# Optimization experiments

Measured on AMD Instinct MI355X. Metric: run time of the kernel, lower is better.

Reference implementation:

```python
import jax, jax.numpy as jnp
import numpy as np

N, E, D_IN, HID, OUT, EDIM, L, NT, ET = 50000, 800000, 128, 128, 128, 32, 3, 2, 3
PUMP = 1
LN_EPS = 1e-5


def setup_inputs() -> dict:
    key = jax.random.key(0)
    ks = jax.random.split(key, 12)
    s = 0.05
    x = jax.random.normal(ks[0], (N, D_IN), jnp.float32)
    edge_index = jax.random.randint(ks[1], (2, E), 0, N, dtype=jnp.int64)
    edge_attr = jax.random.normal(ks[2], (E, EDIM), jnp.float32)
    node_type = jax.random.randint(ks[3], (N,), 0, NT, dtype=jnp.int64)
    edge_type = jax.random.randint(ks[4], (E,), 0, ET, dtype=jnp.int64)
    # per-layer HydroConv params
    node_W = jax.random.normal(ks[5], (L, NT, HID, D_IN), jnp.float32) * s   # per-node-type Linear weight
    node_b = jax.random.normal(ks[6], (L, NT, HID), jnp.float32) * s
    edge_W = jax.random.normal(ks[7], (L, ET, 2, EDIM), jnp.float32) * s     # out dim padded to 2; row 1 only used for pump type
    edge_b = jax.random.normal(ks[8], (L, ET, 2), jnp.float32) * s
    emb = jax.random.normal(ks[9], (L, ET, EDIM), jnp.float32) * s           # edge_type_emb per layer
    ln_g = jnp.ones((L, HID), jnp.float32)
    ln_b = jnp.zeros((L, HID), jnp.float32)
    fc_W = jax.random.normal(ks[10], (OUT, HID), jnp.float32) * s
    fc_b = jnp.zeros((OUT,), jnp.float32)
    return dict(x=x, edge_attr=edge_attr, node_W=node_W, node_b=node_b,
                edge_W=edge_W, edge_b=edge_b, emb=emb, ln_g=ln_g, ln_b=ln_b,
                fc_W=fc_W, fc_b=fc_b, edge_index=edge_index,
                node_type=node_type, edge_type=edge_type)


def _hydro_conv(h, edge_index, edge_attr, node_type, edge_type, nW, nb, eW, eb, emb_l):
    src, dst = edge_index[0], edge_index[1]           # x_j = h[src], x_i = h[dst]
    direction = edge_attr[:, -2:-1]                    # [E,1]
    pump = edge_attr[:, -1:]                           # [E,1]
    ea = edge_attr + emb_l[edge_type]                  # [E,EDIM]
    raw = jnp.einsum('ec,toc->eto', ea, eW) + eb       # [E,ET,2]
    raw = jnp.take_along_axis(raw, edge_type[:, None, None], axis=1)[:, 0]  # [E,2] per-edge-type MLP
    gain = jax.nn.softplus(raw[:, :1])                 # [E,1]
    speed = pump * jnp.where(direction > 0, direction, jnp.ones_like(direction))
    is_pump = (edge_type == PUMP)[:, None]
    gain = jnp.where(is_pump, gain * speed, gain)
    bias = jnp.where(is_pump, raw[:, 1:2] * speed, jnp.zeros_like(gain))
    sign = direction * 2.0 - 1.0
    msg = sign * (gain * (h[src] - h[dst]) + bias)     # [E,C]
    aggr = jax.ops.segment_sum(msg, dst, num_segments=N)  # scatter-add to target nodes
    out = jnp.zeros((N, nW.shape[1]), h.dtype)
    for t in range(NT):                                # per-node-type Linear
        ht = aggr @ nW[t].T + nb[t]
        out = jnp.where((node_type == t)[:, None], ht, out)
    return out


def reference(x, edge_attr, node_W, node_b, edge_W, edge_b, emb, ln_g, ln_b,
              fc_W, fc_b, edge_index, node_type, edge_type):
    h = x
    for l in range(L):
        identity = h
        h = _hydro_conv(h, edge_index, edge_attr, node_type, edge_type,
                        node_W[l], node_b[l], edge_W[l], edge_b[l], emb[l])
        h = jax.nn.relu(h)
        mu = jnp.mean(h, axis=-1, keepdims=True)
        var = jnp.mean(jnp.square(h - mu), axis=-1, keepdims=True)
        h = (h - mu) * jax.lax.rsqrt(var + LN_EPS) * ln_g[l] + ln_b[l]
        if identity.shape == h.shape:                  # residual
            h = h + identity
    return h @ fc_W.T + fc_b
```

## Files before the change

### kernel.cpp

```cpp
#include <hip/hip_runtime.h>
#include <math.h>

#define NN 50000
#define EE 800000
#define D 128
#define EDIM 32
#define LL 3
#define NT 2
#define ET 3
#define NB 196
#define NPAD 50080
#define NTILE 1565
#define NBLKM 392

typedef _Float16 f16x8 __attribute__((ext_vector_type(8)));
typedef float f32x4 __attribute__((ext_vector_type(4)));

__device__ __forceinline__ void cvt8(const float4 u, const float4 v, f16x8& hi, f16x8& lo) {
    float x[8] = {u.x, u.y, u.z, u.w, v.x, v.y, v.z, v.w};
#pragma unroll
    for (int e = 0; e < 8; e++) {
        _Float16 h = (_Float16)x[e];
        hi[e] = h;
        lo[e] = (_Float16)(x[e] - (float)h);
    }
}

__global__ __launch_bounds__(256) void k_pcount(const int* __restrict__ nt, int* __restrict__ pc) {
    __shared__ int s[256];
    int d = blockIdx.x * 256 + threadIdx.x;
    int ind = 0;
    if (d < NN) ind = (nt[d] == 0) ? 1 : 0x10000;
    s[threadIdx.x] = ind;
    __syncthreads();
    for (int st = 128; st; st >>= 1) {
        if (threadIdx.x < st) s[threadIdx.x] += s[threadIdx.x + st];
        __syncthreads();
    }
    if (threadIdx.x == 0) pc[blockIdx.x] = s[0];
}

__global__ __launch_bounds__(256) void k_pscan(const int* __restrict__ pc, int* __restrict__ po,
                                               int* __restrict__ meta) {
    __shared__ int s[256];
    int t = threadIdx.x;
    int v = (t < NB) ? pc[t] : 0;
    s[t] = v;
    __syncthreads();
    for (int st = 1; st < 256; st <<= 1) {
        int add = (t >= st) ? s[t - st] : 0;
        __syncthreads();
        s[t] += add;
        __syncthreads();
    }
    if (t < NB) po[t] = s[t] - v;
    if (t == 0) {
        int tot = s[255];
        meta[3] = ((tot & 0xffff) + 63) & ~63;
    }
}

__global__ __launch_bounds__(256) void k_passign(const int* __restrict__ nt, const int* __restrict__ po,
                                                 const int* __restrict__ meta,
                                                 int* __restrict__ pos, int* __restrict__ inv) {
    __shared__ int s[256];
    int t = threadIdx.x;
    int d = blockIdx.x * 256 + t;
    int ty = (d < NN) ? nt[d] : -1;
    int ind = (ty == 0) ? 1 : ((ty == 1) ? 0x10000 : 0);
    s[t] = ind;
    __syncthreads();
    for (int st = 1; st < 256; st <<= 1) {
        int add = (t >= st) ? s[t - st] : 0;
        __syncthreads();
        s[t] += add;
        __syncthreads();
    }
    if (d >= NN) return;
    int excl = s[t] - ind;
    int pop = po[blockIdx.x];
    int p;
    if (ty == 0) p = (pop & 0xffff) + (excl & 0xffff);
    else         p = meta[3] + (pop >> 16) + (excl >> 16);
    pos[d] = p;
    inv[p] = d;
}

__global__ __launch_bounds__(256) void k_permx(const float* __restrict__ x, const int* __restrict__ pos,
                                               float* __restrict__ h0) {
    int flat = blockIdx.x * 256 + threadIdx.x;
    if (flat >= NN * 32) return;
    int d = flat >> 5, f4 = flat & 31;
    int p = pos[d];
    ((float4*)h0)[(size_t)p * 32 + f4] = ((const float4*)x)[(size_t)d * 32 + f4];
}

__global__ __launch_bounds__(256) void k_hist(const int* __restrict__ dst, int* __restrict__ deg) {
    int e = blockIdx.x * 256 + threadIdx.x;
    if (e < EE) atomicAdd(&deg[dst[e]], 1);
}

__global__ __launch_bounds__(256) void k_scan_bsum(const int* __restrict__ deg, int* __restrict__ bsum) {
    __shared__ int s[256];
    int t = threadIdx.x;
    int d = blockIdx.x * 256 + t;
    s[t] = (d < NN) ? deg[d] : 0;
    __syncthreads();
    for (int st = 128; st > 0; st >>= 1) {
        if (t < st) s[t] += s[t + st];
        __syncthreads();
    }
    if (t == 0) bsum[blockIdx.x] = s[0];
}

__global__ __launch_bounds__(256) void k_scan_boff(const int* __restrict__ bsum, int* __restrict__ boff) {
    __shared__ int s[256];
    int t = threadIdx.x;
    s[t] = (t < NB) ? bsum[t] : 0;
    __syncthreads();
    for (int st = 1; st < 256; st <<= 1) {
        int add = (t >= st) ? s[t - st] : 0;
        __syncthreads();
        s[t] += add;
        __syncthreads();
    }
    if (t < NB) boff[t] = (t == 0) ? 0 : s[t - 1];
}

__global__ __launch_bounds__(256) void k_scan_offs(const int* __restrict__ deg, const int* __restrict__ boff,
                                                   int* __restrict__ offs, int* __restrict__ cur) {
    __shared__ int s[256];
    int t = threadIdx.x;
    int d = blockIdx.x * 256 + t;
    int v = (d < NN) ? deg[d] : 0;
    s[t] = v;
    __syncthreads();
    for (int st = 1; st < 256; st <<= 1) {
        int add = (t >= st) ? s[t - st] : 0;
        __syncthreads();
        s[t] += add;
        __syncthreads();
    }
    if (d < NN) {
        int excl = s[t] - v + boff[blockIdx.x];
        offs[d] = excl;
        cur[d]  = excl;
    }
}

__global__ __launch_bounds__(256) void k_edge(const float* __restrict__ edge_attr,
                                              const float* __restrict__ edge_W,
                                              const float* __restrict__ edge_b,
                                              const float* __restrict__ emb,
                                              const int* __restrict__ ei,
                                              const int* __restrict__ etype,
                                              const int* __restrict__ pos,
                                              int* __restrict__ cur,
                                              float4* __restrict__ esort) {
    __shared__ float eWl[LL * ET * 2 * EDIM];
    __shared__ float ebd[LL * ET * 2];
    int t0 = threadIdx.x;
    for (int i = t0; i < LL * ET * 2 * EDIM; i += 256) eWl[i] = edge_W[i];
    __syncthreads();
    if (t0 < LL * ET * 2) {
        int l = t0 / (ET * 2);
        int rem = t0 % (ET * 2);
        int tt = rem / 2;
        float sum = edge_b[t0];
        const float* em = emb + (l * ET + tt) * EDIM;
        const float* w  = eWl + t0 * EDIM;
        for (int c = 0; c < EDIM; c++) sum += em[c] * w[c];
        ebd[t0] = sum;
    }
    __syncthreads();
    int e = blockIdx.x * 256 + t0;
    if (e >= EE) return;

    float a[EDIM];
    const float4* ap = (const float4*)(edge_attr + (size_t)e * EDIM);
#pragma unroll
    for (int i = 0; i < EDIM / 4; i++) {
        float4 v = ap[i];
        a[4 * i + 0] = v.x; a[4 * i + 1] = v.y; a[4 * i + 2] = v.z; a[4 * i + 3] = v.w;
    }
    int tt = etype[e];
    float dir  = a[EDIM - 2];
    float pump = a[EDIM - 1];
    float sign = dir * 2.f - 1.f;
    float speed = pump * (dir > 0.f ? dir : 1.f);
    int src = ei[e];
    int dst = ei[EE + e];
    int sp = pos[src];
    int p = atomicAdd(&cur[dst], 1);
    float Av[LL], Bv[LL];
#pragma unroll
    for (int l = 0; l < LL; l++) {
        const float* w0 = eWl + ((l * ET + tt) * 2 + 0) * EDIM;
        const float* w1 = w0 + EDIM;
        float r0 = ebd[(l * ET + tt) * 2 + 0];
        float r1 = ebd[(l * ET + tt) * 2 + 1];
#pragma unroll
        for (int c = 0; c < EDIM; c++) { r0 += a[c] * w0[c]; r1 += a[c] * w1[c]; }
        float gain = fmaxf(r0, 0.f) + log1pf(expf(-fabsf(r0)));
        float bias = 0.f;
        if (tt == 1) { gain *= speed; bias = r1 * speed; }
        Av[l] = sign * gain;
        Bv[l] = sign * bias;
    }
    float4 e0 = make_float4(__int_as_float(sp), Av[0], Av[1], Av[2]);
    float4 e1 = make_float4(Bv[0], Bv[1], Bv[2], 0.f);
    esort[(size_t)p * 2 + 0] = e0;
    esort[(size_t)p * 2 + 1] = e1;
}

__global__ __launch_bounds__(256) void k_gather(const float* __restrict__ h,
                                                const int* __restrict__ offs,
                                                const int* __restrict__ deg,
                                                const int* __restrict__ pos,
                                                const float4* __restrict__ esort,
                                                int layer,
                                                float* __restrict__ aggr) {
    __shared__ float4 rbuf[2][32];
    __shared__ float  rsum[2][2];
    int local = threadIdx.x;
    int nb = local >> 7;
    int node = blockIdx.x * 2 + nb;
    int t = local & 127;
    int w = t >> 5;
    int f4 = t & 31;
    int start = offs[node];
    int n = deg[node];
    int p = pos[node];

    float4 acc = make_float4(0.f, 0.f, 0.f, 0.f);
    float sA = 0.f, sB = 0.f;
    for (int k = w; k < n; k += 4) {
        size_t idx = (size_t)(start + k) * 2;
        float4 e0 = esort[idx];
        float4 e1 = esort[idx + 1];
        int sp = __float_as_int(e0.x);
        float A = (layer == 0) ? e0.y : ((layer == 1) ? e0.z : e0.w);
        float B = (layer == 0) ? e1.x : ((layer == 1) ? e1.y : e1.z);
        float4 hv = *(const float4*)&h[(size_t)sp * D + 4 * f4];
        acc.x += A * hv.x; acc.y += A * hv.y; acc.z += A * hv.z; acc.w += A * hv.w;
        sA += A; sB += B;
    }
    acc.x += __shfl_xor(acc.x, 32); acc.y += __shfl_xor(acc.y, 32);
    acc.z += __shfl_xor(acc.z, 32); acc.w += __shfl_xor(acc.w, 32);
    sA += __shfl_xor(sA, 32); sB += __shfl_xor(sB, 32);
    if (((local >> 6) & 1) == 1 && (t & 63) < 32) {
        rbuf[nb][f4] = acc;
        if (f4 == 0) { rsum[nb][0] = sA; rsum[nb][1] = sB; }
    }
    __syncthreads();
    if (((local >> 6) & 1) == 0 && (t & 63) < 32) {
        float4 o = rbuf[nb][f4];
        float sAt = sA + rsum[nb][0];
        float sBt = sB + rsum[nb][1];
        float4 hd = *(const float4*)&h[(size_t)p * D + 4 * f4];
        float4 r;
        r.x = acc.x + o.x - sAt * hd.x + sBt;
        r.y = acc.y + o.y - sAt * hd.y + sBt;
        r.z = acc.z + o.z - sAt * hd.z + sBt;
        r.w = acc.w + o.w - sAt * hd.w + sBt;
        *(float4*)&aggr[(size_t)p * D + 4 * f4] = r;
    }
}

__global__ __launch_bounds__(256) void k_node(const float* __restrict__ aggr,
                                              const float* __restrict__ hprev,
                                              const float* __restrict__ Wg,
                                              const float* __restrict__ bg,
                                              const float* __restrict__ lng,
                                              const float* __restrict__ lnb,
                                              const int* __restrict__ meta,
                                              float* __restrict__ hnext) {
    int wid  = threadIdx.x >> 6;
    int lane = threadIdx.x & 63;
    int w0 = (blockIdx.x * 4 + wid) * 32;
    if (w0 >= NPAD) return;
    int l15 = lane & 15, lg = lane >> 4;
    int tt = (w0 >= meta[3]) ? 1 : 0;
    const float* W = Wg + (size_t)tt * D * D;

    f32x4 acc[2][8];
#pragma unroll
    for (int i = 0; i < 2; i++)
#pragma unroll
        for (int j = 0; j < 8; j++) acc[i][j] = (f32x4){0.f, 0.f, 0.f, 0.f};

#pragma unroll 1
    for (int ks = 0; ks < 4; ks++) {
        int kb = ks * 32 + 8 * lg;
        float4 rA[2][2], rB[8][2];
#pragma unroll
        for (int i = 0; i < 2; i++) {
            const float* p = aggr + (size_t)(w0 + 16 * i + l15) * D + kb;
            rA[i][0] = *(const float4*)p;
            rA[i][1] = *(const float4*)(p + 4);
        }
#pragma unroll
        for (int j = 0; j < 8; j++) {
            const float* p = W + (size_t)(16 * j + l15) * D + kb;
            rB[j][0] = *(const float4*)p;
            rB[j][1] = *(const float4*)(p + 4);
        }
        f16x8 ahi[2], alo[2];
#pragma unroll
        for (int i = 0; i < 2; i++) cvt8(rA[i][0], rA[i][1], ahi[i], alo[i]);
#pragma unroll
        for (int j = 0; j < 8; j++) {
            f16x8 bhi, blo;
            cvt8(rB[j][0], rB[j][1], bhi, blo);
#pragma unroll
            for (int i = 0; i < 2; i++) {
                acc[i][j] = __builtin_amdgcn_mfma_f32_16x16x32_f16(ahi[i], bhi, acc[i][j], 0, 0, 0);
                acc[i][j] = __builtin_amdgcn_mfma_f32_16x16x32_f16(alo[i], bhi, acc[i][j], 0, 0, 0);
                acc[i][j] = __builtin_amdgcn_mfma_f32_16x16x32_f16(ahi[i], blo, acc[i][j], 0, 0, 0);
            }
        }
    }

    float bv[8], gv[8], bb[8];
#pragma unroll
    for (int j = 0; j < 8; j++) {
        int col = 16 * j + l15;
        bv[j] = bg[tt * D + col];
        gv[j] = lng[col];
        bb[j] = lnb[col];
    }
#pragma unroll
    for (int i = 0; i < 2; i++)
#pragma unroll
        for (int j = 0; j < 8; j++)
#pragma unroll
            for (int r = 0; r < 4; r++)
                acc[i][j][r] = fmaxf(acc[i][j][r] + bv[j], 0.f);

    float mu[2][4], rs[2][4];
#pragma unroll
    for (int i = 0; i < 2; i++)
#pragma unroll
        for (int r = 0; r < 4; r++) {
            float s = 0.f, s2 = 0.f;
#pragma unroll
            for (int j = 0; j < 8; j++) { float v = acc[i][j][r]; s += v; s2 += v * v; }
#pragma unroll
            for (int m = 1; m < 16; m <<= 1) { s += __shfl_xor(s, m); s2 += __shfl_xor(s2, m); }
            float mm = s * (1.f / 128.f);
            mu[i][r] = mm;
            rs[i][r] = rsqrtf(s2 * (1.f / 128.f) - mm * mm + 1e-5f);
        }

#pragma unroll
    for (int i = 0; i < 2; i++)
#pragma unroll
        for (int r = 0; r < 4; r++) {
            int row = w0 + 16 * i + 4 * lg + r;
#pragma unroll
            for (int j = 0; j < 8; j++) {
                int col = 16 * j + l15;
                float v = (acc[i][j][r] - mu[i][r]) * rs[i][r] * gv[j] + bb[j]
                          + hprev[(size_t)row * D + col];
                hnext[(size_t)row * D + col] = v;
            }
        }
}

__global__ __launch_bounds__(256) void k_fc(const float* __restrict__ hin,
                                            const float* __restrict__ W,
                                            const float* __restrict__ bias,
                                            const int* __restrict__ inv,
                                            float* __restrict__ out) {
    int wid  = threadIdx.x >> 6;
    int lane = threadIdx.x & 63;
    int w0 = (blockIdx.x * 4 + wid) * 32;
    if (w0 >= NPAD) return;
    int l15 = lane & 15, lg = lane >> 4;

    f32x4 acc[2][8];
#pragma unroll
    for (int i = 0; i < 2; i++)
#pragma unroll
        for (int j = 0; j < 8; j++) acc[i][j] = (f32x4){0.f, 0.f, 0.f, 0.f};

#pragma unroll 1
    for (int ks = 0; ks < 4; ks++) {
        int kb = ks * 32 + 8 * lg;
        float4 rA[2][2], rB[8][2];
#pragma unroll
        for (int i = 0; i < 2; i++) {
            const float* p = hin + (size_t)(w0 + 16 * i + l15) * D + kb;
            rA[i][0] = *(const float4*)p;
            rA[i][1] = *(const float4*)(p + 4);
        }
#pragma unroll
        for (int j = 0; j < 8; j++) {
            const float* p = W + (size_t)(16 * j + l15) * D + kb;
            rB[j][0] = *(const float4*)p;
            rB[j][1] = *(const float4*)(p + 4);
        }
        f16x8 ahi[2], alo[2];
#pragma unroll
        for (int i = 0; i < 2; i++) cvt8(rA[i][0], rA[i][1], ahi[i], alo[i]);
#pragma unroll
        for (int j = 0; j < 8; j++) {
            f16x8 bhi, blo;
            cvt8(rB[j][0], rB[j][1], bhi, blo);
#pragma unroll
            for (int i = 0; i < 2; i++) {
                acc[i][j] = __builtin_amdgcn_mfma_f32_16x16x32_f16(ahi[i], bhi, acc[i][j], 0, 0, 0);
                acc[i][j] = __builtin_amdgcn_mfma_f32_16x16x32_f16(alo[i], bhi, acc[i][j], 0, 0, 0);
                acc[i][j] = __builtin_amdgcn_mfma_f32_16x16x32_f16(ahi[i], blo, acc[i][j], 0, 0, 0);
            }
        }
    }

    float bv[8];
#pragma unroll
    for (int j = 0; j < 8; j++) bv[j] = bias[16 * j + l15];

#pragma unroll
    for (int i = 0; i < 2; i++)
#pragma unroll
        for (int r = 0; r < 4; r++) {
            int row = w0 + 16 * i + 4 * lg + r;
            int orig = inv[row];
            if (orig >= 0) {
#pragma unroll
                for (int j = 0; j < 8; j++)
                    out[(size_t)orig * D + 16 * j + l15] = acc[i][j][r] + bv[j];
            }
        }
}

extern "C" void kernel_launch(void* const* d_in, const int* in_sizes, int n_in,
                              void* d_out, int out_size, void* d_ws, size_t ws_size,
                              hipStream_t stream) {
    const float* x         = (const float*)d_in[0];
    const float* edge_attr = (const float*)d_in[1];
    const float* node_W    = (const float*)d_in[2];
    const float* node_b    = (const float*)d_in[3];
    const float* edge_W    = (const float*)d_in[4];
    const float* edge_b    = (const float*)d_in[5];
    const float* emb       = (const float*)d_in[6];
    const float* ln_g      = (const float*)d_in[7];
    const float* ln_b      = (const float*)d_in[8];
    const float* fc_W      = (const float*)d_in[9];
    const float* fc_b      = (const float*)d_in[10];
    const int*   edge_index = (const int*)d_in[11];
    const int*   node_type  = (const int*)d_in[12];
    const int*   edge_type  = (const int*)d_in[13];
    float* out = (float*)d_out;

    char* w = (char*)d_ws;
    auto alloc = [&](size_t bytes) {
        void* p = (void*)w;
        w += (bytes + 255) & ~(size_t)255;
        return p;
    };
    float*  P     = (float*)alloc((size_t)NPAD * D * 4);
    float*  Q     = (float*)alloc((size_t)NPAD * D * 4);
    float*  G     = (float*)alloc((size_t)NPAD * D * 4);
    float4* esort = (float4*)alloc((size_t)EE * 32);
    int*    pos   = (int*)alloc((size_t)NN * 4);
    int*    inv   = (int*)alloc((size_t)NPAD * 4);
    int*    deg   = (int*)alloc((size_t)NN * 4);
    int*    offs  = (int*)alloc((size_t)NN * 4);
    int*    cur   = (int*)alloc((size_t)NN * 4);
    int*    bsum  = (int*)alloc(256 * 4);
    int*    boff  = (int*)alloc(256 * 4);
    int*    pc    = (int*)alloc(256 * 4);
    int*    po    = (int*)alloc(256 * 4);
    int*    meta  = (int*)alloc(8 * 4);

    hipMemsetAsync(deg, 0, (size_t)NN * 4, stream);
    hipMemsetAsync(inv, 0xFF, (size_t)NPAD * 4, stream);

    k_pcount<<<NB, 256, 0, stream>>>(node_type, pc);
    k_pscan<<<1, 256, 0, stream>>>(pc, po, meta);
    k_passign<<<NB, 256, 0, stream>>>(node_type, po, meta, pos, inv);
    k_permx<<<(NN * 32 + 255) / 256, 256, 0, stream>>>(x, pos, P);

    k_hist<<<(EE + 255) / 256, 256, 0, stream>>>(edge_index + EE, deg);
    k_scan_bsum<<<NB, 256, 0, stream>>>(deg, bsum);
    k_scan_boff<<<1, 256, 0, stream>>>(bsum, boff);
    k_scan_offs<<<NB, 256, 0, stream>>>(deg, boff, offs, cur);
    k_edge<<<(EE + 255) / 256, 256, 0, stream>>>(edge_attr, edge_W, edge_b, emb,
                                                 edge_index, edge_type, pos, cur, esort);

    const float* hin = P;
    float* outs[LL] = {Q, P, Q};
    for (int l = 0; l < LL; l++) {
        k_gather<<<NN / 2, 256, 0, stream>>>(hin, offs, deg, pos, esort, l, G);
        k_node<<<NBLKM, 256, 0, stream>>>(G, hin,
                                          node_W + (size_t)l * NT * D * D,
                                          node_b + (size_t)l * NT * D,
                                          ln_g + (size_t)l * D,
                                          ln_b + (size_t)l * D,
                                          meta, outs[l]);
        hin = outs[l];
    }
    k_fc<<<NBLKM, 256, 0, stream>>>(hin, fc_W, fc_b, inv, out);
}
```

Before: 595.5 us.

## Split edge sort, use per-layer compact edge arrays, halve MFMA row tiles

Edge sorting is split into a separate atomic scatter of edge ids, then a sorted-order edge kernel that reads attributes through the id indirection. It writes per-layer (src, A) float2 arrays instead of a 32-byte record, and pushes the pump-edge bias into a per-node sum with atomics. The gather reads only 8 bytes per edge and unrolls two edges per iteration to overlap the h loads. The node and fc GEMM kernels move from 32-row to 16-row tiles per wave, launching more blocks with fewer registers. The cost is an extra kernel pass, uncoalesced edge_attr reads, float atomics on the bias sums, and the W tile being loaded more often.

```diff
diff --git a/kernel.cpp b/kernel.cpp
--- a/kernel.cpp
+++ b/kernel.cpp
@@ -10,8 +10,8 @@
 #define ET 3
 #define NB 196
 #define NPAD 50080
-#define NTILE 1565
-#define NBLKM 392
+#define NT16 3130
+#define NBLK16 783
 
 typedef _Float16 f16x8 __attribute__((ext_vector_type(8)));
 typedef float f32x4 __attribute__((ext_vector_type(4)));
@@ -148,33 +148,45 @@
     }
 }
 
-__global__ __launch_bounds__(256) void k_edge(const float* __restrict__ edge_attr,
-                                              const float* __restrict__ edge_W,
-                                              const float* __restrict__ edge_b,
-                                              const float* __restrict__ emb,
-                                              const int* __restrict__ ei,
-                                              const int* __restrict__ etype,
-                                              const int* __restrict__ pos,
-                                              int* __restrict__ cur,
-                                              float4* __restrict__ esort) {
-    __shared__ float eWl[LL * ET * 2 * EDIM];
-    __shared__ float ebd[LL * ET * 2];
+__global__ __launch_bounds__(256) void k_scateid(const int* __restrict__ dst,
+                                                 int* __restrict__ cur, int* __restrict__ eid) {
+    int e = blockIdx.x * 256 + threadIdx.x;
+    if (e < EE) {
+        int d = dst[e];
+        int p = atomicAdd(&cur[d], 1);
+        eid[p] = e;
+    }
+}
+
+__global__ __launch_bounds__(256) void k_edge2(const float* __restrict__ edge_attr,
+                                               const float* __restrict__ edge_W,
+                                               const float* __restrict__ edge_b,
+                                               const float* __restrict__ emb,
+                                               const int* __restrict__ ei,
+                                               const int* __restrict__ etype,
+                                               const int* __restrict__ pos,
+                                               const int* __restrict__ eid,
+                                               float2* __restrict__ spA,
+                                               float* __restrict__ sBn) {
+    __shared__ float eWl[18 * 33];
+    __shared__ float ebd[18];
     int t0 = threadIdx.x;
-    for (int i = t0; i < LL * ET * 2 * EDIM; i += 256) eWl[i] = edge_W[i];
-    __syncthreads();
-    if (t0 < LL * ET * 2) {
+    for (int i = t0; i < 18 * EDIM; i += 256) eWl[(i >> 5) * 33 + (i & 31)] = edge_W[i];
+    __syncthreads();
+    if (t0 < 18) {
         int l = t0 / (ET * 2);
         int rem = t0 % (ET * 2);
         int tt = rem / 2;
         float sum = edge_b[t0];
         const float* em = emb + (l * ET + tt) * EDIM;
-        const float* w  = eWl + t0 * EDIM;
+        const float* w  = eWl + t0 * 33;
         for (int c = 0; c < EDIM; c++) sum += em[c] * w[c];
         ebd[t0] = sum;
     }
     __syncthreads();
-    int e = blockIdx.x * 256 + t0;
-    if (e >= EE) return;
+    int p = blockIdx.x * 256 + t0;
+    if (p >= EE) return;
+    int e = eid[p];
 
     float a[EDIM];
     const float4* ap = (const float4*)(edge_attr + (size_t)e * EDIM);
@@ -189,14 +201,12 @@
     float sign = dir * 2.f - 1.f;
     float speed = pump * (dir > 0.f ? dir : 1.f);
     int src = ei[e];
-    int dst = ei[EE + e];
     int sp = pos[src];
-    int p = atomicAdd(&cur[dst], 1);
     float Av[LL], Bv[LL];
 #pragma unroll
     for (int l = 0; l < LL; l++) {
-        const float* w0 = eWl + ((l * ET + tt) * 2 + 0) * EDIM;
-        const float* w1 = w0 + EDIM;
+        const float* w0 = eWl + ((l * ET + tt) * 2 + 0) * 33;
+        const float* w1 = w0 + 33;
         float r0 = ebd[(l * ET + tt) * 2 + 0];
         float r1 = ebd[(l * ET + tt) * 2 + 1];
 #pragma unroll
@@ -207,21 +217,27 @@
         Av[l] = sign * gain;
         Bv[l] = sign * bias;
     }
-    float4 e0 = make_float4(__int_as_float(sp), Av[0], Av[1], Av[2]);
-    float4 e1 = make_float4(Bv[0], Bv[1], Bv[2], 0.f);
-    esort[(size_t)p * 2 + 0] = e0;
-    esort[(size_t)p * 2 + 1] = e1;
+#pragma unroll
+    for (int l = 0; l < LL; l++)
+        spA[(size_t)l * EE + p] = make_float2(__int_as_float(sp), Av[l]);
+    if (tt == 1) {
+        int dst = ei[EE + e];
+        int pd = pos[dst];
+#pragma unroll
+        for (int l = 0; l < LL; l++) atomicAdd(&sBn[l * NPAD + pd], Bv[l]);
+    }
 }
 
 __global__ __launch_bounds__(256) void k_gather(const float* __restrict__ h,
                                                 const int* __restrict__ offs,
                                                 const int* __restrict__ deg,
                                                 const int* __restrict__ pos,
-                                                const float4* __restrict__ esort,
+                                                const float2* __restrict__ spA,
+                                                const float* __restrict__ sBn,
                                                 int layer,
                                                 float* __restrict__ aggr) {
     __shared__ float4 rbuf[2][32];
-    __shared__ float  rsum[2][2];
+    __shared__ float  rsum[2];
     int local = threadIdx.x;
     int nb = local >> 7;
     int node = blockIdx.x * 2 + nb;
@@ -231,32 +247,36 @@
     int start = offs[node];
     int n = deg[node];
     int p = pos[node];
+    const float2* sp_l = spA + (size_t)layer * EE;
 
     float4 acc = make_float4(0.f, 0.f, 0.f, 0.f);
-    float sA = 0.f, sB = 0.f;
-    for (int k = w; k < n; k += 4) {
-        size_t idx = (size_t)(start + k) * 2;
-        float4 e0 = esort[idx];
-        float4 e1 = esort[idx + 1];
-        int sp = __float_as_int(e0.x);
-        float A = (layer == 0) ? e0.y : ((layer == 1) ? e0.z : e0.w);
-        float B = (layer == 0) ? e1.x : ((layer == 1) ? e1.y : e1.z);
-        float4 hv = *(const float4*)&h[(size_t)sp * D + 4 * f4];
-        acc.x += A * hv.x; acc.y += A * hv.y; acc.z += A * hv.z; acc.w += A * hv.w;
-        sA += A; sB += B;
+    float sA = 0.f;
+    for (int k = w; k < n; k += 8) {
+        int k2 = k + 4;
+        float2 sa = sp_l[start + k];
+        float2 sb = (k2 < n) ? sp_l[start + k2] : make_float2(__int_as_float(0), 0.f);
+        int s1 = __float_as_int(sa.x);
+        int s2 = __float_as_int(sb.x);
+        float4 h1 = *(const float4*)&h[(size_t)s1 * D + 4 * f4];
+        float4 h2 = *(const float4*)&h[(size_t)s2 * D + 4 * f4];
+        acc.x += sa.y * h1.x + sb.y * h2.x;
+        acc.y += sa.y * h1.y + sb.y * h2.y;
+        acc.z += sa.y * h1.z + sb.y * h2.z;
+        acc.w += sa.y * h1.w + sb.y * h2.w;
+        sA += sa.y + sb.y;
     }
     acc.x += __shfl_xor(acc.x, 32); acc.y += __shfl_xor(acc.y, 32);
     acc.z += __shfl_xor(acc.z, 32); acc.w += __shfl_xor(acc.w, 32);
-    sA += __shfl_xor(sA, 32); sB += __shfl_xor(sB, 32);
+    sA += __shfl_xor(sA, 32);
     if (((local >> 6) & 1) == 1 && (t & 63) < 32) {
         rbuf[nb][f4] = acc;
-        if (f4 == 0) { rsum[nb][0] = sA; rsum[nb][1] = sB; }
+        if (f4 == 0) rsum[nb] = sA;
     }
     __syncthreads();
     if (((local >> 6) & 1) == 0 && (t & 63) < 32) {
         float4 o = rbuf[nb][f4];
-        float sAt = sA + rsum[nb][0];
-        float sBt = sB + rsum[nb][1];
+        float sAt = sA + rsum[nb];
+        float sBt = sBn[layer * NPAD + p];
         float4 hd = *(const float4*)&h[(size_t)p * D + 4 * f4];
         float4 r;
         r.x = acc.x + o.x - sAt * hd.x + sBt;
@@ -277,47 +297,40 @@
                                               float* __restrict__ hnext) {
     int wid  = threadIdx.x >> 6;
     int lane = threadIdx.x & 63;
-    int w0 = (blockIdx.x * 4 + wid) * 32;
+    int w0 = (blockIdx.x * 4 + wid) * 16;
     if (w0 >= NPAD) return;
     int l15 = lane & 15, lg = lane >> 4;
     int tt = (w0 >= meta[3]) ? 1 : 0;
     const float* W = Wg + (size_t)tt * D * D;
 
-    f32x4 acc[2][8];
-#pragma unroll
-    for (int i = 0; i < 2; i++)
-#pragma unroll
-        for (int j = 0; j < 8; j++) acc[i][j] = (f32x4){0.f, 0.f, 0.f, 0.f};
+    f32x4 acc[8];
+#pragma unroll
+    for (int j = 0; j < 8; j++) acc[j] = (f32x4){0.f, 0.f, 0.f, 0.f};
 
 #pragma unroll 1
     for (int ks = 0; ks < 4; ks++) {
         int kb = ks * 32 + 8 * lg;
-        float4 rA[2][2], rB[8][2];
-#pragma unroll
-        for (int i = 0; i < 2; i++) {
-            const float* p = aggr + (size_t)(w0 + 16 * i + l15) * D + kb;
-            rA[i][0] = *(const float4*)p;
-            rA[i][1] = *(const float4*)(p + 4);
+        float4 rA[2], rB[8][2];
+        {
+            const float* pa = aggr + (size_t)(w0 + l15) * D + kb;
+            rA[0] = *(const float4*)pa;
+            rA[1] = *(const float4*)(pa + 4);
         }
 #pragma unroll
         for (int j = 0; j < 8; j++) {
-            const float* p = W + (size_t)(16 * j + l15) * D + kb;
-            rB[j][0] = *(const float4*)p;
-            rB[j][1] = *(const float4*)(p + 4);
-        }
-        f16x8 ahi[2], alo[2];
-#pragma unroll
-        for (int i = 0; i < 2; i++) cvt8(rA[i][0], rA[i][1], ahi[i], alo[i]);
+            const float* pb = W + (size_t)(16 * j + l15) * D + kb;
+            rB[j][0] = *(const float4*)pb;
+            rB[j][1] = *(const float4*)(pb + 4);
+        }
+        f16x8 ahi, alo;
+        cvt8(rA[0], rA[1], ahi, alo);
 #pragma unroll
         for (int j = 0; j < 8; j++) {
             f16x8 bhi, blo;
             cvt8(rB[j][0], rB[j][1], bhi, blo);
-#pragma unroll
-            for (int i = 0; i < 2; i++) {
-                acc[i][j] = __builtin_amdgcn_mfma_f32_16x16x32_f16(ahi[i], bhi, acc[i][j], 0, 0, 0);
-                acc[i][j] = __builtin_amdgcn_mfma_f32_16x16x32_f16(alo[i], bhi, acc[i][j], 0, 0, 0);
-                acc[i][j] = __builtin_amdgcn_mfma_f32_16x16x32_f16(ahi[i], blo, acc[i][j], 0, 0, 0);
-            }
+            acc[j] = __builtin_amdgcn_mfma_f32_16x16x32_f16(ahi, bhi, acc[j], 0, 0, 0);
+            acc[j] = __builtin_amdgcn_mfma_f32_16x16x32_f16(alo, bhi, acc[j], 0, 0, 0);
+            acc[j] = __builtin_amdgcn_mfma_f32_16x16x32_f16(ahi, blo, acc[j], 0, 0, 0);
         }
     }
 
@@ -330,41 +343,35 @@
         bb[j] = lnb[col];
     }
 #pragma unroll
-    for (int i = 0; i < 2; i++)
-#pragma unroll
-        for (int j = 0; j < 8; j++)
-#pragma unroll
-            for (int r = 0; r < 4; r++)
-                acc[i][j][r] = fmaxf(acc[i][j][r] + bv[j], 0.f);
-
-    float mu[2][4], rs[2][4];
-#pragma unroll
-    for (int i = 0; i < 2; i++)
-#pragma unroll
-        for (int r = 0; r < 4; r++) {
-            float s = 0.f, s2 = 0.f;
-#pragma unroll
-            for (int j = 0; j < 8; j++) { float v = acc[i][j][r]; s += v; s2 += v * v; }
-#pragma unroll
-            for (int m = 1; m < 16; m <<= 1) { s += __shfl_xor(s, m); s2 += __shfl_xor(s2, m); }
-            float mm = s * (1.f / 128.f);
-            mu[i][r] = mm;
-            rs[i][r] = rsqrtf(s2 * (1.f / 128.f) - mm * mm + 1e-5f);
-        }
-
-#pragma unroll
-    for (int i = 0; i < 2; i++)
-#pragma unroll
-        for (int r = 0; r < 4; r++) {
-            int row = w0 + 16 * i + 4 * lg + r;
-#pragma unroll
-            for (int j = 0; j < 8; j++) {
-                int col = 16 * j + l15;
-                float v = (acc[i][j][r] - mu[i][r]) * rs[i][r] * gv[j] + bb[j]
-                          + hprev[(size_t)row * D + col];
-                hnext[(size_t)row * D + col] = v;
-            }
-        }
+    for (int j = 0; j < 8; j++)
+#pragma unroll
+        for (int r = 0; r < 4; r++)
+            acc[j][r] = fmaxf(acc[j][r] + bv[j], 0.f);
+
+    float mu[4], rs[4];
+#pragma unroll
+    for (int r = 0; r < 4; r++) {
+        float s = 0.f, s2 = 0.f;
+#pragma unroll
+        for (int j = 0; j < 8; j++) { float v = acc[j][r]; s += v; s2 += v * v; }
+#pragma unroll
+        for (int m = 1; m < 16; m <<= 1) { s += __shfl_xor(s, m); s2 += __shfl_xor(s2, m); }
+        float mm = s * (1.f / 128.f);
+        mu[r] = mm;
+        rs[r] = rsqrtf(s2 * (1.f / 128.f) - mm * mm + 1e-5f);
+    }
+
+#pragma unroll
+    for (int r = 0; r < 4; r++) {
+        int row = w0 + 4 * lg + r;
+#pragma unroll
+        for (int j = 0; j < 8; j++) {
+            int col = 16 * j + l15;
+            float v = (acc[j][r] - mu[r]) * rs[r] * gv[j] + bb[j]
+                      + hprev[(size_t)row * D + col];
+            hnext[(size_t)row * D + col] = v;
+        }
+    }
 }
 
 __global__ __launch_bounds__(256) void k_fc(const float* __restrict__ hin,
@@ -374,45 +381,38 @@
                                             float* __restrict__ out) {
     int wid  = threadIdx.x >> 6;
     int lane = threadIdx.x & 63;
-    int w0 = (blockIdx.x * 4 + wid) * 32;
+    int w0 = (blockIdx.x * 4 + wid) * 16;
     if (w0 >= NPAD) return;
     int l15 = lane & 15, lg = lane >> 4;
 
-    f32x4 acc[2][8];
-#pragma unroll
-    for (int i = 0; i < 2; i++)
-#pragma unroll
-        for (int j = 0; j < 8; j++) acc[i][j] = (f32x4){0.f, 0.f, 0.f, 0.f};
+    f32x4 acc[8];
+#pragma unroll
+    for (int j = 0; j < 8; j++) acc[j] = (f32x4){0.f, 0.f, 0.f, 0.f};
 
 #pragma unroll 1
     for (int ks = 0; ks < 4; ks++) {
         int kb = ks * 32 + 8 * lg;
-        float4 rA[2][2], rB[8][2];
-#pragma unroll
-        for (int i = 0; i < 2; i++) {
-            const float* p = hin + (size_t)(w0 + 16 * i + l15) * D + kb;
-            rA[i][0] = *(const float4*)p;
-            rA[i][1] = *(const float4*)(p + 4);
+        float4 rA[2], rB[8][2];
+        {
+            const float* pa = hin + (size_t)(w0 + l15) * D + kb;
+            rA[0] = *(const float4*)pa;
+            rA[1] = *(const float4*)(pa + 4);
         }
 #pragma unroll
         for (int j = 0; j < 8; j++) {
-            const float* p = W + (size_t)(16 * j + l15) * D + kb;
-            rB[j][0] = *(const float4*)p;
-            rB[j][1] = *(const float4*)(p + 4);
-        }
-        f16x8 ahi[2], alo[2];
-#pragma unroll
-        for (int i = 0; i < 2; i++) cvt8(rA[i][0], rA[i][1], ahi[i], alo[i]);
+            const float* pb = W + (size_t)(16 * j + l15) * D + kb;
+            rB[j][0] = *(const float4*)pb;
+            rB[j][1] = *(const float4*)(pb + 4);
+        }
+        f16x8 ahi, alo;
+        cvt8(rA[0], rA[1], ahi, alo);
 #pragma unroll
         for (int j = 0; j < 8; j++) {
             f16x8 bhi, blo;
             cvt8(rB[j][0], rB[j][1], bhi, blo);
-#pragma unroll
-            for (int i = 0; i < 2; i++) {
-                acc[i][j] = __builtin_amdgcn_mfma_f32_16x16x32_f16(ahi[i], bhi, acc[i][j], 0, 0, 0);
-                acc[i][j] = __builtin_amdgcn_mfma_f32_16x16x32_f16(alo[i], bhi, acc[i][j], 0, 0, 0);
-                acc[i][j] = __builtin_amdgcn_mfma_f32_16x16x32_f16(ahi[i], blo, acc[i][j], 0, 0, 0);
-            }
+            acc[j] = __builtin_amdgcn_mfma_f32_16x16x32_f16(ahi, bhi, acc[j], 0, 0, 0);
+            acc[j] = __builtin_amdgcn_mfma_f32_16x16x32_f16(alo, bhi, acc[j], 0, 0, 0);
+            acc[j] = __builtin_amdgcn_mfma_f32_16x16x32_f16(ahi, blo, acc[j], 0, 0, 0);
         }
     }
 
@@ -421,17 +421,15 @@
     for (int j = 0; j < 8; j++) bv[j] = bias[16 * j + l15];
 
 #pragma unroll
-    for (int i = 0; i < 2; i++)
-#pragma unroll
-        for (int r = 0; r < 4; r++) {
-            int row = w0 + 16 * i + 4 * lg + r;
-            int orig = inv[row];
-            if (orig >= 0) {
-#pragma unroll
-                for (int j = 0; j < 8; j++)
-                    out[(size_t)orig * D + 16 * j + l15] = acc[i][j][r] + bv[j];
-            }
-        }
+    for (int r = 0; r < 4; r++) {
+        int row = w0 + 4 * lg + r;
+        int orig = inv[row];
+        if (orig >= 0) {
+#pragma unroll
+            for (int j = 0; j < 8; j++)
+                out[(size_t)orig * D + 16 * j + l15] = acc[j][r] + bv[j];
+        }
+    }
 }
 
 extern "C" void kernel_launch(void* const* d_in, const int* in_sizes, int n_in,
@@ -462,7 +460,9 @@
     float*  P     = (float*)alloc((size_t)NPAD * D * 4);
     float*  Q     = (float*)alloc((size_t)NPAD * D * 4);
     float*  G     = (float*)alloc((size_t)NPAD * D * 4);
-    float4* esort = (float4*)alloc((size_t)EE * 32);
+    float2* spA   = (float2*)alloc((size_t)LL * EE * 8);
+    float*  sBn   = (float*)alloc((size_t)LL * NPAD * 4);
+    int*    eid   = (int*)alloc((size_t)EE * 4);
     int*    pos   = (int*)alloc((size_t)NN * 4);
     int*    inv   = (int*)alloc((size_t)NPAD * 4);
     int*    deg   = (int*)alloc((size_t)NN * 4);
@@ -476,6 +476,7 @@
 
     hipMemsetAsync(deg, 0, (size_t)NN * 4, stream);
     hipMemsetAsync(inv, 0xFF, (size_t)NPAD * 4, stream);
+    hipMemsetAsync(sBn, 0, (size_t)LL * NPAD * 4, stream);
 
     k_pcount<<<NB, 256, 0, stream>>>(node_type, pc);
     k_pscan<<<1, 256, 0, stream>>>(pc, po, meta);
@@ -486,20 +487,21 @@
     k_scan_bsum<<<NB, 256, 0, stream>>>(deg, bsum);
     k_scan_boff<<<1, 256, 0, stream>>>(bsum, boff);
     k_scan_offs<<<NB, 256, 0, stream>>>(deg, boff, offs, cur);
-    k_edge<<<(EE + 255) / 256, 256, 0, stream>>>(edge_attr, edge_W, edge_b, emb,
-                                                 edge_index, edge_type, pos, cur, esort);
+    k_scateid<<<(EE + 255) / 256, 256, 0, stream>>>(edge_index + EE, cur, eid);
+    k_edge2<<<(EE + 255) / 256, 256, 0, stream>>>(edge_attr, edge_W, edge_b, emb,
+                                                  edge_index, edge_type, pos, eid, spA, sBn);
 
     const float* hin = P;
     float* outs[LL] = {Q, P, Q};
     for (int l = 0; l < LL; l++) {
-        k_gather<<<NN / 2, 256, 0, stream>>>(hin, offs, deg, pos, esort, l, G);
-        k_node<<<NBLKM, 256, 0, stream>>>(G, hin,
-                                          node_W + (size_t)l * NT * D * D,
-                                          node_b + (size_t)l * NT * D,
-                                          ln_g + (size_t)l * D,
-                                          ln_b + (size_t)l * D,
-                                          meta, outs[l]);
+        k_gather<<<NN / 2, 256, 0, stream>>>(hin, offs, deg, pos, spA, sBn, l, G);
+        k_node<<<NBLK16, 256, 0, stream>>>(G, hin,
+                                           node_W + (size_t)l * NT * D * D,
+                                           node_b + (size_t)l * NT * D,
+                                           ln_g + (size_t)l * D,
+                                           ln_b + (size_t)l * D,
+                                           meta, outs[l]);
         hin = outs[l];
     }
-    k_fc<<<NBLKM, 256, 0, stream>>>(hin, fc_W, fc_b, inv, out);
-}
+    k_fc<<<NBLK16, 256, 0, stream>>>(hin, fc_W, fc_b, inv, out);
+}
```

Measured after the change: 675.5 us. +13.4%, slower.
